# Kernel tuning notes

Measured on AMD Instinct MI355X. Metric: run time of the kernel, lower is better.

## Reference

```python
import jax, jax.numpy as jnp
import numpy as np

L, B, D, H = 4096, 4, 1024, 16
HD = D // H
SCALAR = 700.0


def setup_inputs() -> dict:
    key = jax.random.key(0)
    ks = jax.random.split(key, 9)
    bound = np.sqrt(6.0 / (D + D)).astype(np.float32)  # xavier_uniform for square weights
    def xavier(k):
        return jax.random.uniform(k, (D, D), jnp.float32, -bound, bound)
    return {
        "input_tensor": jax.random.normal(ks[0], (L, B, D), jnp.float32),
        "num_heads": H,
        "Wq": xavier(ks[1]), "bq": jnp.zeros((D,), jnp.float32),
        "Wk": xavier(ks[2]), "bk": jnp.zeros((D,), jnp.float32),
        "Wv": xavier(ks[3]), "bv": jnp.zeros((D,), jnp.float32),
        "Wo": xavier(ks[4]), "bo": jnp.zeros((D,), jnp.float32),
        "scalar": jnp.asarray(SCALAR, jnp.float32),
    }


def reference(input_tensor, num_heads, Wq, bq, Wk, bk, Wv, bv, Wo, bo, scalar):
    l, b, d = input_tensor.shape
    h = num_heads
    hd = d // h
    scaling = hd ** -0.5
    X = jnp.transpose(input_tensor, (1, 0, 2))  # (b, l, d)
    q = (X @ Wq.T + bq) * scaling
    k = X @ Wk.T + bk
    v = X @ Wv.T + bv
    # split heads: (b, l, h*hd) -> (b, h, l, hd)
    q = q.reshape(b, l, h, hd).transpose(0, 2, 1, 3)
    k = k.reshape(b, l, h, hd).transpose(0, 2, 1, 3)
    v = v.reshape(b, l, h, hd).transpose(0, 2, 1, 3)
    # linear attention: (K^T V) then Q @ (...)  -> O(l * hd^2)
    kv = jnp.einsum('bhld,bhle->bhde', k, v)        # (b, h, hd, hd)
    out = jnp.einsum('bhld,bhde->bhle', q, kv) / scalar  # (b, h, l, hd)
    # faithful to einops '(b h) l d -> b l (d h)': feature layout is (hd, h)
    out = out.transpose(0, 2, 3, 1).reshape(b, l, d)  # (b, l, hd*h)
    out = out @ Wo.T + bo
    return jnp.transpose(out, (1, 0, 2))  # (l, b, d)
```

## Files before the change

kernel.cpp:

```cpp
#include <hip/hip_runtime.h>
#include <stdint.h>
#include <stddef.h>

typedef unsigned short ushort_t;
typedef __attribute__((ext_vector_type(8))) short short8;
typedef __attribute__((ext_vector_type(4))) float f32x4;
typedef __attribute__((ext_vector_type(4))) float float4v;

#define L_DIM 4096
#define B_DIM 4
#define D_DIM 1024
#define H_DIM 16
#define HD_DIM 64
#define M_DIM (L_DIM * B_DIM)

__device__ __forceinline__ float bf2f(ushort_t u) {
    union { unsigned int i; float f; } v; v.i = ((unsigned int)u) << 16; return v.f;
}
__device__ __forceinline__ ushort_t f2bf(float f) {
    union { float f; unsigned int i; } v; v.f = f;
    unsigned int r = v.i + 0x7FFFu + ((v.i >> 16) & 1u);
    return (ushort_t)(r >> 16);
}
__device__ __forceinline__ unsigned int pk2(float a, float b) {
    return (unsigned int)f2bf(a) | ((unsigned int)f2bf(b) << 16);
}
__device__ __forceinline__ void gload16(const ushort_t* g, ushort_t* l) {
    __builtin_amdgcn_global_load_lds(
        (const __attribute__((address_space(1))) unsigned int*)g,
        (__attribute__((address_space(3))) unsigned int*)l, 16, 0, 0);
}

union U32x4S8 { unsigned int u[4]; short8 s; };
__device__ __forceinline__ short8 read_frag66(const ushort_t* p) {
    U32x4S8 r;
    r.u[0] = *(const unsigned int*)(p + 0);
    r.u[1] = *(const unsigned int*)(p + 2);
    r.u[2] = *(const unsigned int*)(p + 4);
    r.u[3] = *(const unsigned int*)(p + 6);
    return r.s;
}

__global__ void detect_kernel(const ushort_t* __restrict__ scal, int* __restrict__ flag)
{
    *flag = (scal[0] == 0) ? 1 : 0;
}

__global__ void convert_b_kernel(const void* bq, const void* bk, const void* bv,
                                 const void* bo, float* __restrict__ bias_f,
                                 const int* __restrict__ flag)
{
    int fl = *flag;
    int idx = blockIdx.x * 256 + threadIdx.x;
    int j = idx >> 10, i = idx & 1023;
    const void* p = (j == 0) ? bq : (j == 1) ? bk : (j == 2) ? bv : bo;
    bias_f[idx] = fl ? ((const float*)p)[i] : bf2f(((const ushort_t*)p)[i]);
}

__global__ void convert_w_kernel(const void* Wk, const void* Wv, const void* Wo,
                                 const void* Wq,
                                 ushort_t* __restrict__ Wkc, ushort_t* __restrict__ Wvc,
                                 ushort_t* __restrict__ Wpc, ushort_t* __restrict__ Wqc,
                                 const int* __restrict__ flag)
{
    int fl = *flag;
    int z = blockIdx.z;
    int idx = blockIdx.x * 256 + threadIdx.x;
    const void* src = (z == 0) ? Wk : (z == 1) ? Wv : (z == 2) ? Wo : Wq;
    ushort_t* dst   = (z == 0) ? Wkc : (z == 1) ? Wvc : (z == 2) ? Wpc : Wqc;
    size_t sidx;
    if (z != 2) sidx = (size_t)idx;
    else {
        int n = idx >> 10, f = idx & 1023;
        int hh = f >> 6, e = f & 63;
        sidx = (size_t)n * D_DIM + e * H_DIM + hh;
    }
    dst[idx] = fl ? f2bf(((const float*)src)[sidx]) : ((const ushort_t*)src)[sidx];
}

__global__ void convert_x_kernel(const void* __restrict__ X, ushort_t* __restrict__ Xb,
                                 const int* __restrict__ flag)
{
    int fl = *flag;
    size_t i8 = ((size_t)blockIdx.x * 256 + threadIdx.x) * 8;
    if (fl) {
        const float4v* p = (const float4v*)((const float*)X + i8);
        float4v f0 = p[0], f1 = p[1];
        uint4 u;
        u.x = pk2(f0.x, f0.y); u.y = pk2(f0.z, f0.w);
        u.z = pk2(f1.x, f1.y); u.w = pk2(f1.z, f1.w);
        *(uint4*)(Xb + i8) = u;
    } else {
        *(uint4*)(Xb + i8) = *(const uint4*)((const ushort_t*)X + i8);
    }
}

#define BARRIER() asm volatile("s_barrier" ::: "memory")
#define VMWAIT(N) asm volatile("s_waitcnt vmcnt(" #N ")" ::: "memory")

#define STAGE_A(q, kt, dbuf) {                                                 \
    int kc_ = (kt) < 16 ? (kt) : 15;                                           \
    int row_ = ((w & 4) << 5) + (q) * 32 + ((w & 3) << 3) + lrow8;             \
    gload16(A + (size_t)(a_base + (m0 + row_) * astride) * D_DIM               \
                + kc_ * 64 + kcol,                                             \
            sA + (dbuf) * 16384 + row_ * 64 + lcol8); }

#define STAGE_B(o, kt, dbuf) {                                                 \
    int kc_ = (kt) < 16 ? (kt) : 15;                                           \
    int nr_ = (o) * 64 + (w << 3) + lrow8;                                     \
    gload16(W + (size_t)(n0 + nr_) * D_DIM + kc_ * 64 + kcol,                  \
            sB + (dbuf) * 16384 + nr_ * 64 + lcol8); }

#define PROJ_PHASE(S, STAGE0, STAGE1, WAITSTMT)                                \
  {                                                                            \
    short8 af[2][2];                                                           \
    _Pragma("unroll")                                                          \
    for (int j = 0; j < 2; ++j)                                                \
      _Pragma("unroll")                                                        \
      for (int ks = 0; ks < 2; ++ks)                                           \
        af[j][ks] = *(const short8*)&lAc[(awbase + ((S) * 2 + j) * 16) * 64    \
                                         + ((ks * 32 + q8) ^ swz)];            \
    STAGE0; STAGE1;                                                            \
    BARRIER();                                                                 \
    __builtin_amdgcn_s_setprio(1);                                             \
    _Pragma("unroll")                                                          \
    for (int j = 0; j < 2; ++j)                                                \
      _Pragma("unroll")                                                        \
      for (int nt = 0; nt < 4; ++nt)                                           \
        _Pragma("unroll")                                                      \
        for (int ks = 0; ks < 2; ++ks)                                         \
          acc[(S) * 2 + j][nt] = __builtin_amdgcn_mfma_f32_16x16x32_bf16(      \
              af[j][ks], bf[nt][ks], acc[(S) * 2 + j][nt], 0, 0, 0);           \
    __builtin_amdgcn_s_setprio(0);                                             \
    WAITSTMT;                                                                  \
    BARRIER();                                                                 \
  }

__global__ __launch_bounds__(512) void proj_kernel(
    const ushort_t* __restrict__ A, int a_base0, int a_zstride, int astride,
    const ushort_t* __restrict__ W0, int w_z,
    const float* __restrict__ bias0, int b_z,
    void* __restrict__ out, int o_base0, int o_zstride, int ostride,
    const int* __restrict__ flag, int o_dyn)
{
    extern __shared__ ushort_t smem[];
    ushort_t* sA = smem;
    ushort_t* sB = smem + 32768;

    const int z      = blockIdx.z;
    const int a_base = a_base0 + z * a_zstride;
    const int o_base = o_base0 + z * o_zstride;
    const ushort_t* W = W0 + (size_t)z * w_z * (D_DIM * D_DIM);
    const float* bias = bias0 + z * b_z * D_DIM;
    const int ofl  = o_dyn & *flag;
    const int t    = threadIdx.x;
    const int m0   = blockIdx.x * 256;
    const int n0   = blockIdx.y * 256;
    const int w    = t >> 6;
    const int lane = t & 63;
    const int quad = lane >> 4;
    const int l16  = lane & 15;
    const int wm   = w >> 2;
    const int wn   = w & 3;

    const int lrow8 = lane >> 3;
    const int lcol8 = (lane & 7) * 8;
    const int kcol  = (((lane & 7) ^ lrow8) << 3);

    const int awbase = wm * 128 + l16;
    const int bnbase = wn * 64 + l16;
    const int q8     = quad * 8;
    const int swz    = (l16 & 7) << 3;

    f32x4 acc[8][4];
#pragma unroll
    for (int i = 0; i < 8; i++)
#pragma unroll
        for (int j = 0; j < 4; j++) acc[i][j] = f32x4{0.f, 0.f, 0.f, 0.f};

    STAGE_B(0, 0, 0) STAGE_B(1, 0, 0) STAGE_B(2, 0, 0) STAGE_B(3, 0, 0)
    STAGE_A(0, 0, 0) STAGE_A(1, 0, 0) STAGE_A(2, 0, 0) STAGE_A(3, 0, 0)
    STAGE_B(0, 1, 1) STAGE_B(1, 1, 1)
    VMWAIT(4);
    BARRIER();

    for (int c = 0; c < 16; ++c) {
        const int buf = c & 1, nbuf = buf ^ 1;
        const ushort_t* lAc = sA + buf * 16384;
        const ushort_t* lBc = sB + buf * 16384;

        short8 bf[4][2];
#pragma unroll
        for (int nt = 0; nt < 4; ++nt)
#pragma unroll
            for (int ks = 0; ks < 2; ++ks)
                bf[nt][ks] = *(const short8*)&lBc[(bnbase + nt * 16) * 64
                                                  + ((ks * 32 + q8) ^ swz)];

        PROJ_PHASE(0, STAGE_B(2, c + 1, nbuf), STAGE_B(3, c + 1, nbuf), )
        PROJ_PHASE(1, STAGE_A(0, c + 1, nbuf), STAGE_A(1, c + 1, nbuf), VMWAIT(6))
        PROJ_PHASE(2, STAGE_A(2, c + 1, nbuf), STAGE_A(3, c + 1, nbuf), )
        PROJ_PHASE(3, STAGE_B(0, c + 2, buf),  STAGE_B(1, c + 2, buf),  VMWAIT(4))
    }

#pragma unroll
    for (int mt = 0; mt < 8; ++mt) {
#pragma unroll
        for (int nt = 0; nt < 4; ++nt) {
            const int gn = n0 + wn * 64 + nt * 16 + l16;
            const float bv = bias[gn];
#pragma unroll
            for (int i = 0; i < 4; ++i) {
                const int gm = m0 + wm * 128 + mt * 16 + quad * 4 + i;
                const size_t oidx = (size_t)(o_base + gm * ostride) * D_DIM + gn;
                float val = acc[mt][nt][i] + bv;
                if (ofl) {
                    ((float*)out)[oidx] = val;
                } else {
                    float v2 = __shfl_down(val, 1);
                    if (!(l16 & 1))
                        *(unsigned int*)((ushort_t*)out + oidx) = pk2(val, v2);
                }
            }
        }
    }
}

__global__ __launch_bounds__(256) void proj128_kernel(
    const ushort_t* __restrict__ A, int a_base0, int a_zstride, int astride,
    const ushort_t* __restrict__ W0, int w_z,
    const float* __restrict__ bias0, int b_z,
    void* __restrict__ out, int o_base0, int o_zstride, int ostride,
    const int* __restrict__ flag, int o_dyn)
{
    __shared__ ushort_t lA[128 * 32];
    __shared__ ushort_t lB[128 * 32];
    const int z    = blockIdx.z;
    const int a_base = a_base0 + z * a_zstride;
    const int o_base = o_base0 + z * o_zstride;
    const ushort_t* W = W0 + (size_t)z * w_z * (D_DIM * D_DIM);
    const float* bias = bias0 + z * b_z * D_DIM;
    const int ofl  = o_dyn & *flag;
    const int t    = threadIdx.x;
    const int m0   = blockIdx.x * 128;
    const int n0   = blockIdx.y * 128;
    const int w    = t >> 6;
    const int lane = t & 63;
    const int quad = lane >> 4;
    const int l16  = lane & 15;
    const int wm   = (w >> 1) * 64;
    const int wn   = (w & 1) * 64;

    const int c0 = t, c1 = t + 256;
    const int r0 = c0 >> 2, col0 = (c0 & 3) * 8;
    const int r1 = c1 >> 2, col1 = (c1 & 3) * 8;

    f32x4 acc[4][4];
#pragma unroll
    for (int i = 0; i < 4; i++)
#pragma unroll
        for (int j = 0; j < 4; j++) acc[i][j] = f32x4{0.f, 0.f, 0.f, 0.f};

    for (int k0 = 0; k0 < D_DIM; k0 += 32) {
        __syncthreads();
        gload16(A + (size_t)(a_base + (m0 + r0) * astride) * D_DIM + k0 + col0, &lA[c0 * 8]);
        gload16(A + (size_t)(a_base + (m0 + r1) * astride) * D_DIM + k0 + col1, &lA[c1 * 8]);
        gload16(W + (size_t)(n0 + r0) * D_DIM + k0 + col0, &lB[c0 * 8]);
        gload16(W + (size_t)(n0 + r1) * D_DIM + k0 + col1, &lB[c1 * 8]);
        __syncthreads();
        short8 af[4], bfr[4];
#pragma unroll
        for (int mt = 0; mt < 4; mt++)
            af[mt] = *(const short8*)&lA[(wm + mt * 16 + l16) * 32 + quad * 8];
#pragma unroll
        for (int nt = 0; nt < 4; nt++)
            bfr[nt] = *(const short8*)&lB[(wn + nt * 16 + l16) * 32 + quad * 8];
#pragma unroll
        for (int mt = 0; mt < 4; mt++)
#pragma unroll
            for (int nt = 0; nt < 4; nt++)
                acc[mt][nt] = __builtin_amdgcn_mfma_f32_16x16x32_bf16(
                    af[mt], bfr[nt], acc[mt][nt], 0, 0, 0);
    }

#pragma unroll
    for (int mt = 0; mt < 4; mt++) {
#pragma unroll
        for (int nt = 0; nt < 4; nt++) {
            int gn = n0 + wn + nt * 16 + l16;
            float bv = bias[gn];
#pragma unroll
            for (int i = 0; i < 4; i++) {
                int gm = m0 + wm + mt * 16 + quad * 4 + i;
                size_t oidx = (size_t)(o_base + gm * ostride) * D_DIM + gn;
                float val = acc[mt][nt][i] + bv;
                if (ofl) ((float*)out)[oidx] = val;
                else     ((ushort_t*)out)[oidx] = f2bf(val);
            }
        }
    }
}

__global__ __launch_bounds__(256) void kv_chunk_kernel(
    const ushort_t* __restrict__ kc, const ushort_t* __restrict__ vc,
    float* __restrict__ part, int lps)
{
    __shared__ ushort_t lkT[64 * 32];
    __shared__ ushort_t lvT[64 * 32];
    const int t    = threadIdx.x;
    const int s    = blockIdx.x;
    const int bh   = blockIdx.y;
    const int b    = bh >> 4, h = bh & 15;
    const int w    = t >> 6;
    const int lane = t & 63, quad = lane >> 4, l16 = lane & 15;

    f32x4 acc[4];
#pragma unroll
    for (int i = 0; i < 4; i++) acc[i] = f32x4{0.f, 0.f, 0.f, 0.f};

    const int niter = lps >> 5;
    for (int kt = 0; kt < niter; kt++) {
        int lcur = s * lps + kt * 32;
        __syncthreads();
#pragma unroll
        for (int i = 0; i < 4; i++) {
            int u  = t + 256 * i;
            int l  = u >> 5;
            int dp = u & 31;
            size_t goff = ((size_t)(lcur + l) * B_DIM + b) * D_DIM + h * HD_DIM + dp * 2;
            unsigned int kw = *(const unsigned int*)(kc + goff);
            unsigned int vw = *(const unsigned int*)(vc + goff);
            lkT[(2 * dp) * 32 + l]     = (ushort_t)kw;
            lkT[(2 * dp + 1) * 32 + l] = (ushort_t)(kw >> 16);
            lvT[(2 * dp) * 32 + l]     = (ushort_t)vw;
            lvT[(2 * dp + 1) * 32 + l] = (ushort_t)(vw >> 16);
        }
        __syncthreads();
        short8 af = *(const short8*)&lvT[(w * 16 + l16) * 32 + quad * 8];
#pragma unroll
        for (int dt = 0; dt < 4; dt++) {
            short8 bfr = *(const short8*)&lkT[(dt * 16 + l16) * 32 + quad * 8];
            acc[dt] = __builtin_amdgcn_mfma_f32_16x16x32_bf16(af, bfr, acc[dt], 0, 0, 0);
        }
    }
#pragma unroll
    for (int dt = 0; dt < 4; dt++) {
#pragma unroll
        for (int i = 0; i < 4; i++) {
            int e = w * 16 + quad * 4 + i;
            int d = dt * 16 + l16;
            part[(((size_t)s * 64 + bh) * 64 + e) * 64 + d] += acc[dt][i];
        }
    }
}

__global__ void kv_reduce_kernel(const float* __restrict__ part,
                                 ushort_t* __restrict__ kvT,
                                 const void* __restrict__ scal,
                                 const int* __restrict__ flag)
{
    int fl = *flag;
    float sc = fl ? *(const float*)scal : bf2f(((const ushort_t*)scal)[0]);
    float inv = 1.0f / sc;
    int idx = blockIdx.x * 256 + threadIdx.x;
    float sum = 0.0f;
#pragma unroll
    for (int s = 0; s < 8; s++) sum += part[((size_t)s << 18) + idx];
    kvT[idx] = f2bf(sum * inv);
}

__global__ __launch_bounds__(256) void wfuse_mfma_kernel(
    const ushort_t* __restrict__ Wqc, const ushort_t* __restrict__ kvT,
    ushort_t* __restrict__ WfT)
{
    __shared__ ushort_t lA[256][66];
    __shared__ ushort_t lKV[64][66];
    const int t  = threadIdx.x;
    const int k0 = blockIdx.x * 256;
    const int h  = blockIdx.y, b = blockIdx.z;
    const int w = t >> 6, lane = t & 63, quad = lane >> 4, l16 = lane & 15;
    const ushort_t* wq = Wqc + (size_t)h * 64 * D_DIM + k0;

#pragma unroll
    for (int i = 0; i < 16; ++i) {
        int u = t + 256 * i;
        int kp = u & 127, dp = u >> 7;
        unsigned int w0 = *(const unsigned int*)(wq + (size_t)(2 * dp) * D_DIM + 2 * kp);
        unsigned int w1 = *(const unsigned int*)(wq + (size_t)(2 * dp + 1) * D_DIM + 2 * kp);
        *(unsigned int*)&lA[2 * kp][2 * dp]     = (w0 & 0xffffu) | (w1 << 16);
        *(unsigned int*)&lA[2 * kp + 1][2 * dp] = (w0 >> 16) | (w1 & 0xffff0000u);
    }
    const ushort_t* kvp = kvT + ((size_t)(b * 16 + h) << 12);
#pragma unroll
    for (int i = 0; i < 2; ++i) {
        int u = t + 256 * i;
        int e = u >> 3, d8 = (u & 7) * 8;
        uint4 v = *(const uint4*)(kvp + e * 64 + d8);
        *(unsigned int*)&lKV[e][d8]     = v.x;
        *(unsigned int*)&lKV[e][d8 + 2] = v.y;
        *(unsigned int*)&lKV[e][d8 + 4] = v.z;
        *(unsigned int*)&lKV[e][d8 + 6] = v.w;
    }
    __syncthreads();

    short8 bf[4][2];
#pragma unroll
    for (int nt = 0; nt < 4; ++nt)
#pragma unroll
        for (int ks = 0; ks < 2; ++ks)
            bf[nt][ks] = read_frag66(&lKV[nt * 16 + l16][ks * 32 + quad * 8]);

    f32x4 acc[4][4];
#pragma unroll
    for (int i = 0; i < 4; i++)
#pragma unroll
        for (int j = 0; j < 4; j++) acc[i][j] = f32x4{0.f, 0.f, 0.f, 0.f};

#pragma unroll
    for (int mt = 0; mt < 4; ++mt) {
        const int krow = w * 64 + mt * 16 + l16;
        short8 af0 = read_frag66(&lA[krow][quad * 8]);
        short8 af1 = read_frag66(&lA[krow][32 + quad * 8]);
#pragma unroll
        for (int nt = 0; nt < 4; ++nt) {
            acc[mt][nt] = __builtin_amdgcn_mfma_f32_16x16x32_bf16(
                af0, bf[nt][0], acc[mt][nt], 0, 0, 0);
            acc[mt][nt] = __builtin_amdgcn_mfma_f32_16x16x32_bf16(
                af1, bf[nt][1], acc[mt][nt], 0, 0, 0);
        }
    }

#pragma unroll
    for (int mt = 0; mt < 4; ++mt) {
#pragma unroll
        for (int nt = 0; nt < 4; ++nt) {
            const int gf = h * 64 + nt * 16 + l16;
#pragma unroll
            for (int i = 0; i < 4; ++i) {
                const int gk = k0 + w * 64 + mt * 16 + quad * 4 + i;
                float val = 0.125f * acc[mt][nt][i];
                float v2 = __shfl_down(val, 1);
                if (!(l16 & 1))
                    *(unsigned int*)(WfT + ((size_t)b * 1024 + gk) * D_DIM + gf)
                        = pk2(val, v2);
            }
        }
    }
}

__global__ void bias_fuse_kernel(const float* __restrict__ bq_f,
                                 const ushort_t* __restrict__ kvT,
                                 float* __restrict__ bfused)
{
    int idx = blockIdx.x * 256 + threadIdx.x;
    int b = idx >> 10, h = (idx >> 6) & 15, e = idx & 63;
    const ushort_t* kvp = kvT + ((size_t)(b * 16 + h) << 12) + e * 64;
    float s = 0.f;
#pragma unroll
    for (int d = 0; d < 64; d++) s += bf2f(kvp[d]) * bq_f[h * 64 + d];
    bfused[idx] = 0.125f * s;
}

__global__ void bias2_kernel(const ushort_t* __restrict__ Wpc,
                             const float* __restrict__ bfused,
                             const float* __restrict__ bo_f,
                             float* __restrict__ b2)
{
    int idx = blockIdx.x * 256 + threadIdx.x;
    int b = idx >> 10, n = idx & 1023;
    const ushort_t* wr = Wpc + (size_t)n * D_DIM;
    const float* bf = bfused + b * 1024;
    float s = 0.f;
    for (int f = 0; f < 1024; f++) s += bf2f(wr[f]) * bf[f];
    b2[idx] = s + bo_f[n];
}

extern "C" void kernel_launch(void* const* d_in, const int* in_sizes, int n_in,
                              void* d_out, int out_size, void* d_ws, size_t ws_size,
                              hipStream_t stream)
{
    const void* X    = d_in[0];
    const void* Wq   = d_in[2];
    const void* bq   = d_in[3];
    const void* Wk   = d_in[4];
    const void* bk   = d_in[5];
    const void* Wv   = d_in[6];
    const void* bv   = d_in[7];
    const void* Wo   = d_in[8];
    const void* bo   = d_in[9];
    const void* scal = d_in[10];

    (void)hipFuncSetAttribute((const void*)proj_kernel,
                              hipFuncAttributeMaxDynamicSharedMemorySize, 131072);

    char* ws = (char*)d_ws;
    int*      flag   = (int*)(ws + 0);
    float*    bias_f = (float*)(ws + 1024);
    float*    bfused = (float*)(ws + 32768);
    float*    b2     = (float*)(ws + 65536);
    float*    bias_z = (float*)(ws + 98304);
    ushort_t* Wkc    = (ushort_t*)(ws + 131072);
    ushort_t* Wvc    = (ushort_t*)(ws + 2228224);
    ushort_t* Wpc    = (ushort_t*)(ws + 4325376);
    ushort_t* kvT    = (ushort_t*)(ws + 6422528);
    float*    part   = (float*)(ws + 6946816);
    ushort_t* Xb     = (ushort_t*)(ws + 15335424);
    ushort_t* kvbuf  = (ushort_t*)(ws + 48889856);
    ushort_t* kc     = kvbuf;
    ushort_t* vc     = kvbuf + (size_t)8192 * D_DIM;
    ushort_t* WfT    = kvbuf;
    ushort_t* W2     = kvbuf + (size_t)4194304;
    ushort_t* Wqc    = (ushort_t*)(ws + 82444288);

    detect_kernel<<<1, 1, 0, stream>>>((const ushort_t*)scal, flag);
    convert_b_kernel<<<16, 256, 0, stream>>>(bq, bk, bv, bo, bias_f, flag);
    convert_w_kernel<<<dim3(4096, 1, 4), 256, 0, stream>>>(Wk, Wv, Wo, Wq,
                                                           Wkc, Wvc, Wpc, Wqc, flag);
    convert_x_kernel<<<8192, 256, 0, stream>>>(X, Xb, flag);
    hipMemsetAsync(part, 0, 8388608, stream);
    hipMemsetAsync(bias_z, 0, 4096, stream);

    for (int c = 0; c < 2; c++) {
        proj_kernel<<<dim3(32, 4, 2), 512, 131072, stream>>>(
            Xb, c * 8192, 0, 1,
            Wkc, 1,
            bias_f + 1024, 1,
            kvbuf, 0, 8192, 1,
            flag, 0);
        kv_chunk_kernel<<<dim3(8, 64), 256, 0, stream>>>(kc, vc, part, 256);
    }
    kv_reduce_kernel<<<1024, 256, 0, stream>>>(part, kvT, scal, flag);

    wfuse_mfma_kernel<<<dim3(4, 16, 4), 256, 0, stream>>>(Wqc, kvT, WfT);
    bias_fuse_kernel<<<16, 256, 0, stream>>>(bias_f, kvT, bfused);
    bias2_kernel<<<16, 256, 0, stream>>>(Wpc, bfused, bias_f + 3072, b2);

    proj128_kernel<<<dim3(8, 8, 4), 256, 0, stream>>>(
        Wpc, 0, 0, 1,
        WfT, 1,
        bias_z, 0,
        W2, 0, 1024, 1,
        flag, 0);

    proj_kernel<<<dim3(16, 4, 4), 512, 131072, stream>>>(
        Xb, 0, 1, 4,
        W2, 1,
        b2, 1,
        d_out, 0, 1, 4,
        flag, 1);
}
```

Before: 417.0 us.

## Stage projection GEMM tiles through registers instead of direct global-to-LDS loads

Replaces the direct global-to-LDS (gload16) staging in the projection GEMM with plain global loads into registers, followed by swizzled ds_write stores that are interleaved with the MFMA phases. The explicit vmcnt waits are removed, and the load/store schedule is reorganized so that A is prefetched one K-step ahead and B two steps ahead. Launch bounds now request 2 blocks per CU. This adds register pressure and extra LDS write instructions, and may cause spills under the tighter occupancy bound.

```diff
diff --git a/kernel.cpp b/kernel.cpp
--- a/kernel.cpp
+++ b/kernel.cpp
@@ -96,22 +96,24 @@
 }
 
 #define BARRIER() asm volatile("s_barrier" ::: "memory")
-#define VMWAIT(N) asm volatile("s_waitcnt vmcnt(" #N ")" ::: "memory")
-
-#define STAGE_A(q, kt, dbuf) {                                                 \
+
+#define GLD_A(reg, q, kt) {                                                    \
     int kc_ = (kt) < 16 ? (kt) : 15;                                           \
-    int row_ = ((w & 4) << 5) + (q) * 32 + ((w & 3) << 3) + lrow8;             \
-    gload16(A + (size_t)(a_base + (m0 + row_) * astride) * D_DIM               \
-                + kc_ * 64 + kcol,                                             \
-            sA + (dbuf) * 16384 + row_ * 64 + lcol8); }
-
-#define STAGE_B(o, kt, dbuf) {                                                 \
+    reg = *(const uint4*)(A + (size_t)(a_base + (m0 + (q) * 64) * astride)     \
+                                  * D_DIM + kc_ * 64 + alane); }
+
+#define GLD_B(reg, q, kt) {                                                    \
     int kc_ = (kt) < 16 ? (kt) : 15;                                           \
-    int nr_ = (o) * 64 + (w << 3) + lrow8;                                     \
-    gload16(W + (size_t)(n0 + nr_) * D_DIM + kc_ * 64 + kcol,                  \
-            sB + (dbuf) * 16384 + nr_ * 64 + lcol8); }
-
-#define PROJ_PHASE(S, STAGE0, STAGE1, WAITSTMT)                                \
+    reg = *(const uint4*)(W + (size_t)(n0 + (q) * 64) * D_DIM                  \
+                              + kc_ * 64 + blane); }
+
+#define DSW_A(q, dbuf, reg) {                                                  \
+    *(uint4*)(sA + (dbuf) * 16384 + (q) * 4096 + lwl) = reg; }
+
+#define DSW_B(q, dbuf, reg) {                                                  \
+    *(uint4*)(sB + (dbuf) * 16384 + (q) * 4096 + lwl) = reg; }
+
+#define PROJ_PHASE(S, WR0, WR1, IS0, IS1)                                      \
   {                                                                            \
     short8 af[2][2];                                                           \
     _Pragma("unroll")                                                          \
@@ -120,7 +122,7 @@
       for (int ks = 0; ks < 2; ++ks)                                           \
         af[j][ks] = *(const short8*)&lAc[(awbase + ((S) * 2 + j) * 16) * 64    \
                                          + ((ks * 32 + q8) ^ swz)];            \
-    STAGE0; STAGE1;                                                            \
+    WR0 WR1 IS0 IS1                                                            \
     BARRIER();                                                                 \
     __builtin_amdgcn_s_setprio(1);                                             \
     _Pragma("unroll")                                                          \
@@ -132,11 +134,10 @@
           acc[(S) * 2 + j][nt] = __builtin_amdgcn_mfma_f32_16x16x32_bf16(      \
               af[j][ks], bf[nt][ks], acc[(S) * 2 + j][nt], 0, 0, 0);           \
     __builtin_amdgcn_s_setprio(0);                                             \
-    WAITSTMT;                                                                  \
     BARRIER();                                                                 \
   }
 
-__global__ __launch_bounds__(512) void proj_kernel(
+__global__ __launch_bounds__(512, 2) void proj_kernel(
     const ushort_t* __restrict__ A, int a_base0, int a_zstride, int astride,
     const ushort_t* __restrict__ W0, int w_z,
     const float* __restrict__ bias0, int b_z,
@@ -163,9 +164,11 @@
     const int wm   = w >> 2;
     const int wn   = w & 3;
 
-    const int lrow8 = lane >> 3;
-    const int lcol8 = (lane & 7) * 8;
-    const int kcol  = (((lane & 7) ^ lrow8) << 3);
+    const int trow = t >> 3;
+    const int tg   = t & 7;
+    const int alane = trow * astride * D_DIM + tg * 8;
+    const int blane = trow * D_DIM + tg * 8;
+    const int lwl   = trow * 64 + ((tg ^ (trow & 7)) * 8);
 
     const int awbase = wm * 128 + l16;
     const int bnbase = wn * 64 + l16;
@@ -178,11 +181,14 @@
 #pragma unroll
         for (int j = 0; j < 4; j++) acc[i][j] = f32x4{0.f, 0.f, 0.f, 0.f};
 
-    STAGE_B(0, 0, 0) STAGE_B(1, 0, 0) STAGE_B(2, 0, 0) STAGE_B(3, 0, 0)
-    STAGE_A(0, 0, 0) STAGE_A(1, 0, 0) STAGE_A(2, 0, 0) STAGE_A(3, 0, 0)
-    STAGE_B(0, 1, 1) STAGE_B(1, 1, 1)
-    VMWAIT(4);
-    BARRIER();
+    uint4 hA0, hA1, hA2, hA3, hB0, hB1, hB2, hB3;
+
+    GLD_B(hB0, 0, 0) GLD_B(hB1, 1, 0) GLD_B(hB2, 2, 0) GLD_B(hB3, 3, 0)
+    GLD_A(hA0, 0, 0) GLD_A(hA1, 1, 0) GLD_A(hA2, 2, 0) GLD_A(hA3, 3, 0)
+    DSW_B(0, 0, hB0) DSW_B(1, 0, hB1) DSW_B(2, 0, hB2) DSW_B(3, 0, hB3)
+    DSW_A(0, 0, hA0) DSW_A(1, 0, hA1) DSW_A(2, 0, hA2) DSW_A(3, 0, hA3)
+    GLD_B(hB0, 0, 1) GLD_B(hB1, 1, 1) GLD_B(hB2, 2, 1) GLD_B(hB3, 3, 1)
+    __syncthreads();
 
     for (int c = 0; c < 16; ++c) {
         const int buf = c & 1, nbuf = buf ^ 1;
@@ -197,10 +203,14 @@
                 bf[nt][ks] = *(const short8*)&lBc[(bnbase + nt * 16) * 64
                                                   + ((ks * 32 + q8) ^ swz)];
 
-        PROJ_PHASE(0, STAGE_B(2, c + 1, nbuf), STAGE_B(3, c + 1, nbuf), )
-        PROJ_PHASE(1, STAGE_A(0, c + 1, nbuf), STAGE_A(1, c + 1, nbuf), VMWAIT(6))
-        PROJ_PHASE(2, STAGE_A(2, c + 1, nbuf), STAGE_A(3, c + 1, nbuf), )
-        PROJ_PHASE(3, STAGE_B(0, c + 2, buf),  STAGE_B(1, c + 2, buf),  VMWAIT(4))
+        PROJ_PHASE(0, DSW_B(0, nbuf, hB0), DSW_B(1, nbuf, hB1),
+                      GLD_A(hA0, 0, c + 1), GLD_A(hA1, 1, c + 1))
+        PROJ_PHASE(1, DSW_B(2, nbuf, hB2), DSW_B(3, nbuf, hB3),
+                      GLD_A(hA2, 2, c + 1), GLD_A(hA3, 3, c + 1))
+        PROJ_PHASE(2, DSW_A(0, nbuf, hA0), DSW_A(1, nbuf, hA1),
+                      GLD_B(hB0, 0, c + 2), GLD_B(hB1, 1, c + 2))
+        PROJ_PHASE(3, DSW_A(2, nbuf, hA2), DSW_A(3, nbuf, hA3),
+                      GLD_B(hB2, 2, c + 2), GLD_B(hB3, 3, c + 2))
     }
 
 #pragma unroll
```

Result: slower. 428.7 us (+2.8%).

## Compute KV via X^T X Gram matrix instead of projecting full K and V

Applied to the files above, without the earlier changes.

Replaces the per-token K/V projection and chunked K^T V reduction with an algebraic form. It computes the Gram matrix G = X^T X per batch, multiplies it by Wv, then takes the per-head diagonal blocks with Wk, and adds bias terms from column sums of X. This swaps roughly 2·L·D·D flops of projection per batch for a D·D·L Gram product, and removes the fp32 partial buffer, its memset and the reduce kernel. It also drops the flag-detect kernel by checking the scalar format inline, and adds a transposed copy of X plus swizzled LDS in the 128-tile GEMM.

```diff
diff --git a/kernel.cpp b/kernel.cpp
--- a/kernel.cpp
+++ b/kernel.cpp
@@ -12,7 +12,6 @@
 #define D_DIM 1024
 #define H_DIM 16
 #define HD_DIM 64
-#define M_DIM (L_DIM * B_DIM)
 
 __device__ __forceinline__ float bf2f(ushort_t u) {
     union { unsigned int i; float f; } v; v.i = ((unsigned int)u) << 16; return v.f;
@@ -24,6 +23,9 @@
 }
 __device__ __forceinline__ unsigned int pk2(float a, float b) {
     return (unsigned int)f2bf(a) | ((unsigned int)f2bf(b) << 16);
+}
+__device__ __forceinline__ int scal_is_f32(const void* scal) {
+    return (((const ushort_t*)scal)[0] == 0) ? 1 : 0;
 }
 __device__ __forceinline__ void gload16(const ushort_t* g, ushort_t* l) {
     __builtin_amdgcn_global_load_lds(
@@ -41,16 +43,11 @@
     return r.s;
 }
 
-__global__ void detect_kernel(const ushort_t* __restrict__ scal, int* __restrict__ flag)
-{
-    *flag = (scal[0] == 0) ? 1 : 0;
-}
-
 __global__ void convert_b_kernel(const void* bq, const void* bk, const void* bv,
                                  const void* bo, float* __restrict__ bias_f,
-                                 const int* __restrict__ flag)
-{
-    int fl = *flag;
+                                 const void* __restrict__ scal)
+{
+    int fl = scal_is_f32(scal);
     int idx = blockIdx.x * 256 + threadIdx.x;
     int j = idx >> 10, i = idx & 1023;
     const void* p = (j == 0) ? bq : (j == 1) ? bk : (j == 2) ? bv : bo;
@@ -61,9 +58,9 @@
                                  const void* Wq,
                                  ushort_t* __restrict__ Wkc, ushort_t* __restrict__ Wvc,
                                  ushort_t* __restrict__ Wpc, ushort_t* __restrict__ Wqc,
-                                 const int* __restrict__ flag)
-{
-    int fl = *flag;
+                                 const void* __restrict__ scal)
+{
+    int fl = scal_is_f32(scal);
     int z = blockIdx.z;
     int idx = blockIdx.x * 256 + threadIdx.x;
     const void* src = (z == 0) ? Wk : (z == 1) ? Wv : (z == 2) ? Wo : Wq;
@@ -78,21 +75,63 @@
     dst[idx] = fl ? f2bf(((const float*)src)[sidx]) : ((const ushort_t*)src)[sidx];
 }
 
-__global__ void convert_x_kernel(const void* __restrict__ X, ushort_t* __restrict__ Xb,
-                                 const int* __restrict__ flag)
-{
-    int fl = *flag;
-    size_t i8 = ((size_t)blockIdx.x * 256 + threadIdx.x) * 8;
+__global__ void convert_xt_kernel(const void* __restrict__ X, ushort_t* __restrict__ Xb,
+                                  ushort_t* __restrict__ XbT, const void* __restrict__ scal)
+{
+    __shared__ ushort_t lT[64][66];
+    const int fl = scal_is_f32(scal);
+    const int lt = blockIdx.x, dt = blockIdx.y, b = blockIdx.z;
+    const int t = threadIdx.x;
+    const int r = t >> 2, seg = t & 3;
+    const size_t grow = (((size_t)(lt * 64 + r) * 4 + b) * 1024) + dt * 64 + seg * 16;
+    uint4 u0, u1;
     if (fl) {
-        const float4v* p = (const float4v*)((const float*)X + i8);
-        float4v f0 = p[0], f1 = p[1];
-        uint4 u;
-        u.x = pk2(f0.x, f0.y); u.y = pk2(f0.z, f0.w);
-        u.z = pk2(f1.x, f1.y); u.w = pk2(f1.z, f1.w);
-        *(uint4*)(Xb + i8) = u;
+        const float4v* p = (const float4v*)((const float*)X + grow);
+        float4v f0 = p[0], f1 = p[1], f2 = p[2], f3 = p[3];
+        u0.x = pk2(f0.x, f0.y); u0.y = pk2(f0.z, f0.w);
+        u0.z = pk2(f1.x, f1.y); u0.w = pk2(f1.z, f1.w);
+        u1.x = pk2(f2.x, f2.y); u1.y = pk2(f2.z, f2.w);
+        u1.z = pk2(f3.x, f3.y); u1.w = pk2(f3.z, f3.w);
     } else {
-        *(uint4*)(Xb + i8) = *(const uint4*)((const ushort_t*)X + i8);
-    }
+        const uint4* p = (const uint4*)((const ushort_t*)X + grow);
+        u0 = p[0]; u1 = p[1];
+    }
+    uint4* xo = (uint4*)(Xb + grow);
+    xo[0] = u0; xo[1] = u1;
+    unsigned int* ld = (unsigned int*)&lT[r][seg * 16];
+    ld[0] = u0.x; ld[1] = u0.y; ld[2] = u0.z; ld[3] = u0.w;
+    ld[4] = u1.x; ld[5] = u1.y; ld[6] = u1.z; ld[7] = u1.w;
+    __syncthreads();
+    const int d = t >> 2, ls = t & 3;
+    union { ushort_t us[16]; uint4 u4[2]; } pk_;
+#pragma unroll
+    for (int j = 0; j < 16; ++j) pk_.us[j] = lT[ls * 16 + j][d];
+    uint4* to = (uint4*)(XbT + ((size_t)b * 1024 + dt * 64 + d) * 4096 + lt * 64 + ls * 16);
+    to[0] = pk_.u4[0]; to[1] = pk_.u4[1];
+}
+
+__global__ void s_kernel(const ushort_t* __restrict__ Xb, float* __restrict__ s)
+{
+    const int b = blockIdx.x;
+    const int d = blockIdx.y * 256 + threadIdx.x;
+    float acc = 0.f;
+    const ushort_t* p = Xb + (size_t)b * 1024 + d;
+#pragma unroll 4
+    for (int l = 0; l < 4096; ++l) acc += bf2f(p[(size_t)l * 4096]);
+    s[b * 1024 + d] = acc;
+}
+
+__global__ void svec_kernel(const ushort_t* __restrict__ Wkc, const ushort_t* __restrict__ Wvc,
+                            const float* __restrict__ s, float* __restrict__ wsk,
+                            float* __restrict__ wsv)
+{
+    int idx = blockIdx.x * 256 + threadIdx.x;
+    int which = idx >> 12, b = (idx >> 10) & 3, n = idx & 1023;
+    const ushort_t* wr = (which ? Wvc : Wkc) + (size_t)n * 1024;
+    const float* sb = s + b * 1024;
+    float acc = 0.f;
+    for (int q = 0; q < 1024; ++q) acc += bf2f(wr[q]) * sb[q];
+    (which ? wsv : wsk)[b * 1024 + n] = acc;
 }
 
 #define BARRIER() asm volatile("s_barrier" ::: "memory")
@@ -141,7 +180,7 @@
     const ushort_t* __restrict__ W0, int w_z,
     const float* __restrict__ bias0, int b_z,
     void* __restrict__ out, int o_base0, int o_zstride, int ostride,
-    const int* __restrict__ flag, int o_dyn)
+    const void* __restrict__ scal, int o_dyn)
 {
     extern __shared__ ushort_t smem[];
     ushort_t* sA = smem;
@@ -152,7 +191,7 @@
     const int o_base = o_base0 + z * o_zstride;
     const ushort_t* W = W0 + (size_t)z * w_z * (D_DIM * D_DIM);
     const float* bias = bias0 + z * b_z * D_DIM;
-    const int ofl  = o_dyn & *flag;
+    const int ofl  = o_dyn & scal_is_f32(scal);
     const int t    = threadIdx.x;
     const int m0   = blockIdx.x * 256;
     const int n0   = blockIdx.y * 256;
@@ -226,21 +265,21 @@
     }
 }
 
-__global__ __launch_bounds__(256) void proj128_kernel(
+__global__ __launch_bounds__(256) void proj128k_kernel(
     const ushort_t* __restrict__ A, int a_base0, int a_zstride, int astride,
-    const ushort_t* __restrict__ W0, int w_z,
+    const ushort_t* __restrict__ W0, size_t w_ze, int wstride,
     const float* __restrict__ bias0, int b_z,
     void* __restrict__ out, int o_base0, int o_zstride, int ostride,
-    const int* __restrict__ flag, int o_dyn)
+    const void* __restrict__ scal, int o_dyn, int kdim)
 {
     __shared__ ushort_t lA[128 * 32];
     __shared__ ushort_t lB[128 * 32];
     const int z    = blockIdx.z;
     const int a_base = a_base0 + z * a_zstride;
     const int o_base = o_base0 + z * o_zstride;
-    const ushort_t* W = W0 + (size_t)z * w_z * (D_DIM * D_DIM);
-    const float* bias = bias0 + z * b_z * D_DIM;
-    const int ofl  = o_dyn & *flag;
+    const ushort_t* W = W0 + (size_t)z * w_ze;
+    const float* bias = bias0 + (b_z > 0 ? z * b_z * D_DIM : 0);
+    const int ofl  = o_dyn & scal_is_f32(scal);
     const int t    = threadIdx.x;
     const int m0   = blockIdx.x * 128;
     const int n0   = blockIdx.y * 128;
@@ -252,8 +291,11 @@
     const int wn   = (w & 1) * 64;
 
     const int c0 = t, c1 = t + 256;
-    const int r0 = c0 >> 2, col0 = (c0 & 3) * 8;
-    const int r1 = c1 >> 2, col1 = (c1 & 3) * 8;
+    const int r0 = c0 >> 2, g0 = c0 & 3;
+    const int r1 = c1 >> 2, g1 = c1 & 3;
+    const int col0 = ((g0 ^ (r0 & 3)) * 8);
+    const int col1 = ((g1 ^ (r1 & 3)) * 8);
+    const int rsw  = l16 & 3;
 
     f32x4 acc[4][4];
 #pragma unroll
@@ -261,20 +303,20 @@
 #pragma unroll
         for (int j = 0; j < 4; j++) acc[i][j] = f32x4{0.f, 0.f, 0.f, 0.f};
 
-    for (int k0 = 0; k0 < D_DIM; k0 += 32) {
+    for (int k0 = 0; k0 < kdim; k0 += 32) {
         __syncthreads();
         gload16(A + (size_t)(a_base + (m0 + r0) * astride) * D_DIM + k0 + col0, &lA[c0 * 8]);
         gload16(A + (size_t)(a_base + (m0 + r1) * astride) * D_DIM + k0 + col1, &lA[c1 * 8]);
-        gload16(W + (size_t)(n0 + r0) * D_DIM + k0 + col0, &lB[c0 * 8]);
-        gload16(W + (size_t)(n0 + r1) * D_DIM + k0 + col1, &lB[c1 * 8]);
+        gload16(W + (size_t)(n0 + r0) * wstride + k0 + col0, &lB[c0 * 8]);
+        gload16(W + (size_t)(n0 + r1) * wstride + k0 + col1, &lB[c1 * 8]);
         __syncthreads();
         short8 af[4], bfr[4];
 #pragma unroll
         for (int mt = 0; mt < 4; mt++)
-            af[mt] = *(const short8*)&lA[(wm + mt * 16 + l16) * 32 + quad * 8];
+            af[mt] = *(const short8*)&lA[(wm + mt * 16 + l16) * 32 + ((quad ^ rsw) * 8)];
 #pragma unroll
         for (int nt = 0; nt < 4; nt++)
-            bfr[nt] = *(const short8*)&lB[(wn + nt * 16 + l16) * 32 + quad * 8];
+            bfr[nt] = *(const short8*)&lB[(wn + nt * 16 + l16) * 32 + ((quad ^ rsw) * 8)];
 #pragma unroll
         for (int mt = 0; mt < 4; mt++)
 #pragma unroll
@@ -288,85 +330,94 @@
 #pragma unroll
         for (int nt = 0; nt < 4; nt++) {
             int gn = n0 + wn + nt * 16 + l16;
-            float bv = bias[gn];
+            float bv = (b_z < 0) ? 0.0f : bias[gn];
 #pragma unroll
             for (int i = 0; i < 4; i++) {
                 int gm = m0 + wm + mt * 16 + quad * 4 + i;
                 size_t oidx = (size_t)(o_base + gm * ostride) * D_DIM + gn;
                 float val = acc[mt][nt][i] + bv;
-                if (ofl) ((float*)out)[oidx] = val;
-                else     ((ushort_t*)out)[oidx] = f2bf(val);
+                if (ofl) {
+                    ((float*)out)[oidx] = val;
+                } else {
+                    float v2 = __shfl_down(val, 1);
+                    if (!(l16 & 1))
+                        *(unsigned int*)((ushort_t*)out + oidx) = pk2(val, v2);
+                }
             }
         }
     }
 }
 
-__global__ __launch_bounds__(256) void kv_chunk_kernel(
-    const ushort_t* __restrict__ kc, const ushort_t* __restrict__ vc,
-    float* __restrict__ part, int lps)
-{
-    __shared__ ushort_t lkT[64 * 32];
-    __shared__ ushort_t lvT[64 * 32];
-    const int t    = threadIdx.x;
-    const int s    = blockIdx.x;
-    const int bh   = blockIdx.y;
-    const int b    = bh >> 4, h = bh & 15;
-    const int w    = t >> 6;
-    const int lane = t & 63, quad = lane >> 4, l16 = lane & 15;
+__global__ __launch_bounds__(256) void kv_diag_kernel(
+    const ushort_t* __restrict__ P, const ushort_t* __restrict__ Wkc,
+    const float* __restrict__ bias_f, const float* __restrict__ wsk,
+    const float* __restrict__ wsv, ushort_t* __restrict__ kvT,
+    const void* __restrict__ scal)
+{
+    __shared__ ushort_t lA[64 * 64];
+    __shared__ ushort_t lB[64 * 64];
+    const int bh = blockIdx.x, b = bh >> 4, h = bh & 15;
+    const int t = threadIdx.x;
+    const int w = t >> 6, lane = t & 63, quad = lane >> 4, l16 = lane & 15;
+    const int fl = scal_is_f32(scal);
+    const float sc = fl ? *(const float*)scal : bf2f(((const ushort_t*)scal)[0]);
+    const float inv = 1.0f / sc;
+
+    const int g0 = t, g1 = t + 256;
+    const int r0 = g0 >> 3, gc0 = g0 & 7, col0 = ((gc0 ^ (r0 & 7)) * 8);
+    const int r1 = g1 >> 3, gc1 = g1 & 7, col1 = ((gc1 ^ (r1 & 7)) * 8);
+    const ushort_t* Ab = P + (size_t)b * 1048576 + (size_t)(h * 64) * 1024;
+    const ushort_t* Bb = Wkc + (size_t)(h * 64) * 1024;
+    const int rsw = l16 & 7;
 
     f32x4 acc[4];
 #pragma unroll
     for (int i = 0; i < 4; i++) acc[i] = f32x4{0.f, 0.f, 0.f, 0.f};
 
-    const int niter = lps >> 5;
-    for (int kt = 0; kt < niter; kt++) {
-        int lcur = s * lps + kt * 32;
+    for (int kt = 0; kt < 16; ++kt) {
+        const int k0 = kt * 64;
         __syncthreads();
-#pragma unroll
-        for (int i = 0; i < 4; i++) {
-            int u  = t + 256 * i;
-            int l  = u >> 5;
-            int dp = u & 31;
-            size_t goff = ((size_t)(lcur + l) * B_DIM + b) * D_DIM + h * HD_DIM + dp * 2;
-            unsigned int kw = *(const unsigned int*)(kc + goff);
-            unsigned int vw = *(const unsigned int*)(vc + goff);
-            lkT[(2 * dp) * 32 + l]     = (ushort_t)kw;
-            lkT[(2 * dp + 1) * 32 + l] = (ushort_t)(kw >> 16);
-            lvT[(2 * dp) * 32 + l]     = (ushort_t)vw;
-            lvT[(2 * dp + 1) * 32 + l] = (ushort_t)(vw >> 16);
+        gload16(Ab + (size_t)r0 * 1024 + k0 + col0, &lA[g0 * 8]);
+        gload16(Ab + (size_t)r1 * 1024 + k0 + col1, &lA[g1 * 8]);
+        gload16(Bb + (size_t)r0 * 1024 + k0 + col0, &lB[g0 * 8]);
+        gload16(Bb + (size_t)r1 * 1024 + k0 + col1, &lB[g1 * 8]);
+        __syncthreads();
+        short8 af[2], bfr[4][2];
+#pragma unroll
+        for (int ks = 0; ks < 2; ++ks)
+            af[ks] = *(const short8*)&lA[(w * 16 + l16) * 64 + (((ks * 4 + quad) ^ rsw) * 8)];
+#pragma unroll
+        for (int nt = 0; nt < 4; ++nt)
+#pragma unroll
+            for (int ks = 0; ks < 2; ++ks)
+                bfr[nt][ks] = *(const short8*)&lB[(nt * 16 + l16) * 64
+                                                  + (((ks * 4 + quad) ^ rsw) * 8)];
+#pragma unroll
+        for (int nt = 0; nt < 4; ++nt)
+#pragma unroll
+            for (int ks = 0; ks < 2; ++ks)
+                acc[nt] = __builtin_amdgcn_mfma_f32_16x16x32_bf16(
+                    af[ks], bfr[nt][ks], acc[nt], 0, 0, 0);
+    }
+
+    const float* bkf  = bias_f + 1024 + h * 64;
+    const float* bvf  = bias_f + 2048 + h * 64;
+    const float* wskb = wsk + b * 1024 + h * 64;
+    const float* wsvb = wsv + b * 1024 + h * 64;
+#pragma unroll
+    for (int nt = 0; nt < 4; ++nt) {
+        const int d = nt * 16 + l16;
+        const float bkd = bkf[d], wskd = wskb[d];
+#pragma unroll
+        for (int i = 0; i < 4; ++i) {
+            const int e = w * 16 + quad * 4 + i;
+            float val = (acc[nt][i] + wsvb[e] * bkd + bvf[e] * wskd
+                         + 4096.0f * bvf[e] * bkd) * inv;
+            float v2 = __shfl_down(val, 1);
+            if (!(l16 & 1))
+                *(unsigned int*)(kvT + ((size_t)bh << 12) + e * 64 + d) = pk2(val, v2);
         }
-        __syncthreads();
-        short8 af = *(const short8*)&lvT[(w * 16 + l16) * 32 + quad * 8];
-#pragma unroll
-        for (int dt = 0; dt < 4; dt++) {
-            short8 bfr = *(const short8*)&lkT[(dt * 16 + l16) * 32 + quad * 8];
-            acc[dt] = __builtin_amdgcn_mfma_f32_16x16x32_bf16(af, bfr, acc[dt], 0, 0, 0);
-        }
-    }
-#pragma unroll
-    for (int dt = 0; dt < 4; dt++) {
-#pragma unroll
-        for (int i = 0; i < 4; i++) {
-            int e = w * 16 + quad * 4 + i;
-            int d = dt * 16 + l16;
-            part[(((size_t)s * 64 + bh) * 64 + e) * 64 + d] += acc[dt][i];
-        }
-    }
-}
-
-__global__ void kv_reduce_kernel(const float* __restrict__ part,
-                                 ushort_t* __restrict__ kvT,
-                                 const void* __restrict__ scal,
-                                 const int* __restrict__ flag)
-{
-    int fl = *flag;
-    float sc = fl ? *(const float*)scal : bf2f(((const ushort_t*)scal)[0]);
-    float inv = 1.0f / sc;
-    int idx = blockIdx.x * 256 + threadIdx.x;
-    float sum = 0.0f;
-#pragma unroll
-    for (int s = 0; s < 8; s++) sum += part[((size_t)s << 18) + idx];
-    kvT[idx] = f2bf(sum * inv);
+    }
 }
 
 __global__ __launch_bounds__(256) void wfuse_mfma_kernel(
@@ -482,8 +533,8 @@
     const void* X    = d_in[0];
     const void* Wq   = d_in[2];
     const void* bq   = d_in[3];
+    const void* bk   = d_in[5];
     const void* Wk   = d_in[4];
-    const void* bk   = d_in[5];
     const void* Wv   = d_in[6];
     const void* bv   = d_in[7];
     const void* Wo   = d_in[8];
@@ -494,58 +545,63 @@
                               hipFuncAttributeMaxDynamicSharedMemorySize, 131072);
 
     char* ws = (char*)d_ws;
-    int*      flag   = (int*)(ws + 0);
     float*    bias_f = (float*)(ws + 1024);
     float*    bfused = (float*)(ws + 32768);
     float*    b2     = (float*)(ws + 65536);
-    float*    bias_z = (float*)(ws + 98304);
-    ushort_t* Wkc    = (ushort_t*)(ws + 131072);
-    ushort_t* Wvc    = (ushort_t*)(ws + 2228224);
-    ushort_t* Wpc    = (ushort_t*)(ws + 4325376);
-    ushort_t* kvT    = (ushort_t*)(ws + 6422528);
-    float*    part   = (float*)(ws + 6946816);
-    ushort_t* Xb     = (ushort_t*)(ws + 15335424);
-    ushort_t* kvbuf  = (ushort_t*)(ws + 48889856);
-    ushort_t* kc     = kvbuf;
-    ushort_t* vc     = kvbuf + (size_t)8192 * D_DIM;
-    ushort_t* WfT    = kvbuf;
-    ushort_t* W2     = kvbuf + (size_t)4194304;
-    ushort_t* Wqc    = (ushort_t*)(ws + 82444288);
-
-    detect_kernel<<<1, 1, 0, stream>>>((const ushort_t*)scal, flag);
-    convert_b_kernel<<<16, 256, 0, stream>>>(bq, bk, bv, bo, bias_f, flag);
+    float*    s      = (float*)(ws + 98304);
+    float*    wsk    = (float*)(ws + 114688);
+    float*    wsv    = (float*)(ws + 147456);
+    ushort_t* kvT    = (ushort_t*)(ws + 1048576);
+    ushort_t* Wkc    = (ushort_t*)(ws + 2097152);
+    ushort_t* Wvc    = (ushort_t*)(ws + 4194304);
+    ushort_t* Wpc    = (ushort_t*)(ws + 6291456);
+    ushort_t* Wqc    = (ushort_t*)(ws + 8388608);
+    ushort_t* G      = (ushort_t*)(ws + 10485760);
+    ushort_t* Xb     = (ushort_t*)(ws + 18874368);
+    ushort_t* XbT    = (ushort_t*)(ws + 52428800);
+    ushort_t* P      = (ushort_t*)(ws + 52428800);
+    ushort_t* WfT    = (ushort_t*)(ws + 60817408);
+    ushort_t* W2     = (ushort_t*)(ws + 69206016);
+
+    convert_b_kernel<<<16, 256, 0, stream>>>(bq, bk, bv, bo, bias_f, scal);
     convert_w_kernel<<<dim3(4096, 1, 4), 256, 0, stream>>>(Wk, Wv, Wo, Wq,
-                                                           Wkc, Wvc, Wpc, Wqc, flag);
-    convert_x_kernel<<<8192, 256, 0, stream>>>(X, Xb, flag);
-    hipMemsetAsync(part, 0, 8388608, stream);
-    hipMemsetAsync(bias_z, 0, 4096, stream);
-
-    for (int c = 0; c < 2; c++) {
-        proj_kernel<<<dim3(32, 4, 2), 512, 131072, stream>>>(
-            Xb, c * 8192, 0, 1,
-            Wkc, 1,
-            bias_f + 1024, 1,
-            kvbuf, 0, 8192, 1,
-            flag, 0);
-        kv_chunk_kernel<<<dim3(8, 64), 256, 0, stream>>>(kc, vc, part, 256);
-    }
-    kv_reduce_kernel<<<1024, 256, 0, stream>>>(part, kvT, scal, flag);
+                                                           Wkc, Wvc, Wpc, Wqc, scal);
+    convert_xt_kernel<<<dim3(64, 16, 4), 256, 0, stream>>>(X, Xb, XbT, scal);
+    s_kernel<<<dim3(4, 4), 256, 0, stream>>>(Xb, s);
+
+    proj128k_kernel<<<dim3(8, 8, 4), 256, 0, stream>>>(
+        XbT, 0, 4096, 4,
+        XbT, (size_t)4194304, 4096,
+        bias_f, -1,
+        G, 0, 1024, 1,
+        scal, 0, 4096);
+
+    svec_kernel<<<32, 256, 0, stream>>>(Wkc, Wvc, s, wsk, wsv);
+
+    proj128k_kernel<<<dim3(8, 8, 4), 256, 0, stream>>>(
+        Wvc, 0, 0, 1,
+        G, (size_t)1048576, 1024,
+        bias_f, -1,
+        P, 0, 1024, 1,
+        scal, 0, 1024);
+
+    kv_diag_kernel<<<64, 256, 0, stream>>>(P, Wkc, bias_f, wsk, wsv, kvT, scal);
 
     wfuse_mfma_kernel<<<dim3(4, 16, 4), 256, 0, stream>>>(Wqc, kvT, WfT);
     bias_fuse_kernel<<<16, 256, 0, stream>>>(bias_f, kvT, bfused);
     bias2_kernel<<<16, 256, 0, stream>>>(Wpc, bfused, bias_f + 3072, b2);
 
-    proj128_kernel<<<dim3(8, 8, 4), 256, 0, stream>>>(
+    proj128k_kernel<<<dim3(8, 8, 4), 256, 0, stream>>>(
         Wpc, 0, 0, 1,
-        WfT, 1,
-        bias_z, 0,
+        WfT, (size_t)1048576, 1024,
+        bias_f, -1,
         W2, 0, 1024, 1,
-        flag, 0);
+        scal, 0, 1024);
 
     proj_kernel<<<dim3(16, 4, 4), 512, 131072, stream>>>(
         Xb, 0, 1, 4,
         W2, 1,
         b2, 1,
         d_out, 0, 1, 4,
-        flag, 1);
-}
+        scal, 1);
+}
```

Result: slower. 801.1 us (+92.1%).
